# Kernel tuning notes

Hardware: AMD Instinct MI355X
Metric: run time of the kernel (lower is better)

Reference implementation:

```python
import jax, jax.numpy as jnp
import numpy as np

N, E = 100000, 1600000
IN_F, H, D = 128, 4, 32
NEG_SLOPE = 0.2


def setup_inputs() -> dict:
    key = jax.random.key(0)
    k1, k2, k3, k4, k5, k6 = jax.random.split(key, 6)
    feat = jax.random.normal(k1, (N, IN_F), dtype=jnp.float32)
    src = jax.random.randint(k2, (E,), 0, N, dtype=jnp.int32)
    dst = jax.random.randint(k3, (E,), 0, N, dtype=jnp.int32)
    # learned params (xavier-ish scale)
    W = jax.random.normal(k4, (IN_F, H * D), dtype=jnp.float32) * (2.0 / (IN_F + H * D)) ** 0.5
    attn_l = jax.random.normal(k5, (H, D), dtype=jnp.float32) * 0.1
    attn_r = jax.random.normal(k6, (H, D), dtype=jnp.float32) * 0.1
    return {"feat": feat, "W": W, "attn_l": attn_l, "attn_r": attn_r, "src": src, "dst": dst}


def reference(feat, W, attn_l, attn_r, src, dst):
    n = feat.shape[0]
    # linear projection: [N, H, D]
    ft = (feat @ W).reshape(n, H, D)
    # per-node attention logits: [N, H]
    el = jnp.einsum('nhd,hd->nh', ft, attn_l)
    er = jnp.einsum('nhd,hd->nh', ft, attn_r)
    # per-edge score e_ij = LeakyReLU(el[src] + er[dst]): [E, H]
    e = el[src] + er[dst]
    e = jnp.where(e > 0, e, NEG_SLOPE * e)
    # edge softmax over incoming edges of each destination node
    emax = jax.ops.segment_max(e, dst, num_segments=n)        # [N, H]
    emax = jnp.where(jnp.isfinite(emax), emax, 0.0)           # guard isolated nodes
    ex = jnp.exp(e - emax[dst])                               # [E, H]
    denom = jax.ops.segment_sum(ex, dst, num_segments=n)      # [N, H]
    denom = jnp.where(denom > 0, denom, 1.0)
    a = ex / denom[dst]                                       # [E, H]
    # weighted gather-scatter aggregation: sum_j a_ij * ft_j
    m = ft[src] * a[:, :, None]                               # [E, H, D]
    rst = jax.ops.segment_sum(m, dst, num_segments=n)         # [N, H, D]
    return rst
```

## Files before the change

kernel.cpp:

```cpp
#include <hip/hip_runtime.h>
#include <hip/hip_fp16.h>

constexpr int IN_F = 128;
constexpr int NH   = 4;
constexpr int ND   = 32;
constexpr int HD   = 128;
constexpr float NEG_SLOPE = 0.2f;
constexpr int NBLK   = 256;
constexpr int BSH    = 7;
constexpr int BNODES = 1 << BSH;

using short8 = __attribute__((ext_vector_type(8))) short;
using f32x4  = __attribute__((ext_vector_type(4))) float;
using f32x2  = __attribute__((ext_vector_type(2))) float;

__device__ inline unsigned bf16b(float f) {
  unsigned u = __float_as_uint(f);
  return (u + 0x7FFFu + ((u >> 16) & 1u)) >> 16;
}

__global__ __launch_bounds__(256) void k_chist(
    const int* __restrict__ dst, int* __restrict__ cnt, int ne, int nbuk,
    const float* __restrict__ W, const float* __restrict__ attn_l,
    const float* __restrict__ attn_r, unsigned* __restrict__ wtx) {
  const int t = threadIdx.x;
  const int item = blockIdx.x * 256 + t;
  if (item < 144 * 16) {
    const int r = item >> 4, s = item & 15;
    const int k0 = s * 8;
    unsigned pk[4];
    if (r < HD) {
#pragma unroll
      for (int j2 = 0; j2 < 4; ++j2) {
        const unsigned lo = bf16b(W[(size_t)(k0 + 2 * j2) * HD + r]);
        const unsigned hi = bf16b(W[(size_t)(k0 + 2 * j2 + 1) * HD + r]);
        pk[j2] = lo | (hi << 16);
      }
    } else if (r < HD + 8) {
      const int j8 = r - HD;
      const int h = j8 & 3;
      const float* av = (j8 < 4 ? attn_l : attn_r) + h * ND;
      float sums[8];
#pragma unroll
      for (int j = 0; j < 8; ++j) {
        const float4* wv = (const float4*)&W[(size_t)(k0 + j) * HD + h * ND];
        const float4* a4 = (const float4*)av;
        float sum = 0.f;
#pragma unroll
        for (int c4 = 0; c4 < ND / 4; ++c4) {
          const float4 w = wv[c4], a = a4[c4];
          sum += w.x * a.x + w.y * a.y + w.z * a.z + w.w * a.w;
        }
        sums[j] = sum;
      }
#pragma unroll
      for (int j2 = 0; j2 < 4; ++j2)
        pk[j2] = bf16b(sums[2 * j2]) | (bf16b(sums[2 * j2 + 1]) << 16);
    } else {
      pk[0] = pk[1] = pk[2] = pk[3] = 0;
    }
    *(uint4*)&wtx[r * 64 + ((s ^ (r & 7)) << 2)] =
        make_uint4(pk[0], pk[1], pk[2], pk[3]);
  }
  __shared__ int hist[1024];
  for (int b = t; b < nbuk; b += 256) hist[b] = 0;
  __syncthreads();
  const int chunk = (ne + NBLK - 1) / NBLK;
  const int start = blockIdx.x * chunk;
  const int end = min(start + chunk, ne);
  for (int e = start + t; e < end; e += 256)
    atomicAdd(&hist[dst[e] >> BSH], 1);
  __syncthreads();
  for (int b = t; b < nbuk; b += 256) cnt[b * NBLK + blockIdx.x] = hist[b];
}

__global__ __launch_bounds__(256) void k_gemm(
    const float* __restrict__ feat, const unsigned* __restrict__ wtx,
    unsigned* __restrict__ ftb2, float* __restrict__ el, float* __restrict__ er,
    int n) {
  __shared__ unsigned sB[144 * 64];
  const int t = threadIdx.x;
  {
    const uint4* wx = (const uint4*)wtx;
    uint4* sx = (uint4*)sB;
    for (int it = t; it < 144 * 16; it += 256) sx[it] = wx[it];
  }
  __syncthreads();

  const int lane = t & 63;
  const int wv   = t >> 6;
  const int r0   = blockIdx.x * 128 + wv * 32;
  if (r0 >= n) return;
  const int lrow = lane & 15;
  const int lk   = lane >> 4;

  f32x4 acc[2][9];
#pragma unroll
  for (int st = 0; st < 2; ++st)
#pragma unroll
    for (int ct = 0; ct < 9; ++ct) acc[st][ct] = (f32x4)0.f;

#pragma unroll
  for (int ks = 0; ks < 4; ++ks) {
    short8 b[9];
#pragma unroll
    for (int ct = 0; ct < 9; ++ct) {
      const int row = ct * 16 + lrow;
      const int slot = ks * 4 + lk;
      b[ct] = *(const short8*)&sB[row * 64 + ((slot ^ (row & 7)) << 2)];
    }
#pragma unroll
    for (int st = 0; st < 2; ++st) {
      int arow = r0 + st * 16 + lrow;
      arow = arow < n ? arow : n - 1;
      const float* ap = feat + (size_t)arow * IN_F + ks * 32 + lk * 8;
      const float4 f0 = *(const float4*)ap;
      const float4 f1 = *(const float4*)(ap + 4);
      short8 a;
      a[0] = (short)bf16b(f0.x); a[1] = (short)bf16b(f0.y);
      a[2] = (short)bf16b(f0.z); a[3] = (short)bf16b(f0.w);
      a[4] = (short)bf16b(f1.x); a[5] = (short)bf16b(f1.y);
      a[6] = (short)bf16b(f1.z); a[7] = (short)bf16b(f1.w);
#pragma unroll
      for (int ct = 0; ct < 9; ++ct)
        acc[st][ct] = __builtin_amdgcn_mfma_f32_16x16x32_bf16(a, b[ct], acc[st][ct], 0, 0, 0);
    }
  }

#pragma unroll
  for (int st = 0; st < 2; ++st) {
#pragma unroll
    for (int i = 0; i < 4; ++i) {
      const int r = r0 + st * 16 + lk * 4 + i;
      if (r >= n) continue;
#pragma unroll
      for (int ct = 0; ct < 4; ++ct) {
        const unsigned pk = bf16b(acc[st][ct][i]) | (bf16b(acc[st][ct + 4][i]) << 16);
        ftb2[(size_t)r * 64 + ct * 16 + lrow] = pk;
      }
      if (lrow < 4)      el[r * NH + lrow]     = acc[st][8][i];
      else if (lrow < 8) er[r * NH + lrow - 4] = acc[st][8][i];
    }
  }
}

__global__ __launch_bounds__(256) void k_scan1(
    const int* __restrict__ in, int* __restrict__ pexcl,
    int* __restrict__ bsum, int len) {
  const int t = threadIdx.x;
  const int base = blockIdx.x * 1024 + t * 4;
  int v0 = base + 0 < len ? in[base + 0] : 0;
  int v1 = base + 1 < len ? in[base + 1] : 0;
  int v2 = base + 2 < len ? in[base + 2] : 0;
  int v3 = base + 3 < len ? in[base + 3] : 0;
  const int s = v0 + v1 + v2 + v3;
  const int lane = t & 63, w = t >> 6;
  int x = s;
#pragma unroll
  for (int off = 1; off < 64; off <<= 1) {
    int y = __shfl_up(x, off);
    if (lane >= off) x += y;
  }
  __shared__ int ws[4];
  if (lane == 63) ws[w] = x;
  __syncthreads();
  int woff = 0;
  for (int i = 0; i < w; ++i) woff += ws[i];
  int run = woff + x - s;
  if (base + 0 < len) { pexcl[base + 0] = run; run += v0; }
  if (base + 1 < len) { pexcl[base + 1] = run; run += v1; }
  if (base + 2 < len) { pexcl[base + 2] = run; run += v2; }
  if (base + 3 < len) { pexcl[base + 3] = run; run += v3; }
  if (t == 0) bsum[blockIdx.x] = ws[0] + ws[1] + ws[2] + ws[3];
}

__global__ __launch_bounds__(256) void k_scan23(
    const int* __restrict__ pexcl, const int* __restrict__ bsum,
    int* __restrict__ outv, int B, int len) {
  const int t = threadIdx.x;
  const int s = t < B ? bsum[t] : 0;
  const int lane = t & 63, w = t >> 6;
  int x = s;
#pragma unroll
  for (int off = 1; off < 64; off <<= 1) {
    int y = __shfl_up(x, off);
    if (lane >= off) x += y;
  }
  __shared__ int ws[4];
  __shared__ int sboff[256];
  if (lane == 63) ws[w] = x;
  __syncthreads();
  int woff = 0;
  for (int i = 0; i < w; ++i) woff += ws[i];
  sboff[t] = woff + x - s;
  __syncthreads();
  const int myoff = sboff[blockIdx.x];
  const int base = blockIdx.x * 1024 + t * 4;
#pragma unroll
  for (int j = 0; j < 4; ++j)
    if (base + j < len) outv[base + j] = pexcl[base + j] + myoff;
}

__global__ __launch_bounds__(256) void k_part(
    const int* __restrict__ src, const int* __restrict__ dst,
    const int* __restrict__ scanned, int2* __restrict__ pair, int ne, int nbuk) {
  __shared__ int cur[1024];
  const int t = threadIdx.x;
  for (int b = t; b < nbuk; b += 256) cur[b] = scanned[b * NBLK + blockIdx.x];
  __syncthreads();
  const int chunk = (ne + NBLK - 1) / NBLK;
  const int start = blockIdx.x * chunk;
  const int end = min(start + chunk, ne);
  for (int e = start + t; e < end; e += 256) {
    const int d = dst[e];
    const int pos = atomicAdd(&cur[d >> BSH], 1);
    pair[pos] = make_int2(src[e], d);
  }
}

__global__ __launch_bounds__(256) void k_fsort(
    const int2* __restrict__ pair, const int* __restrict__ scanned,
    const float* __restrict__ el, const float* __restrict__ er,
    int* __restrict__ offsets, int4* __restrict__ rec,
    int n, int ne, int nbuk) {
  const int b = blockIdx.x;
  const int t = threadIdx.x;
  const int base = scanned[b * NBLK];
  const int endp = (b + 1 < nbuk) ? scanned[(b + 1) * NBLK] : ne;
  __shared__ int hist[BNODES];
  __shared__ int cur[BNODES];
  __shared__ int ws2[2];
  if (t < BNODES) hist[t] = 0;
  __syncthreads();
  for (int i = base + t; i < endp; i += 256)
    atomicAdd(&hist[pair[i].y & (BNODES - 1)], 1);
  __syncthreads();
  int x = 0, v = 0;
  if (t < BNODES) {
    v = hist[t];
    x = v;
    const int lane = t & 63;
#pragma unroll
    for (int off = 1; off < 64; off <<= 1) {
      int y = __shfl_up(x, off);
      if (lane >= off) x += y;
    }
    if (lane == 63) ws2[t >> 6] = x;
  }
  __syncthreads();
  if (t < BNODES) {
    if (t >= 64) x += ws2[0];
    const int excl = base + x - v;
    cur[t] = excl;
    const int node = (b << BSH) + t;
    if (node < n) offsets[node] = excl;
  }
  if (b == 0 && t == 0) offsets[n] = ne;
  __syncthreads();
  for (int i = base + t; i < endp; i += 256) {
    const int2 pr = pair[i];
    const int pos = atomicAdd(&cur[pr.y & (BNODES - 1)], 1);
    const float4 l = *(const float4*)(el + (size_t)pr.x * NH);
    const float4 r = *(const float4*)(er + (size_t)pr.y * NH);
    float e0 = l.x + r.x, e1 = l.y + r.y, e2 = l.z + r.z, e3 = l.w + r.w;
    e0 = e0 > 0.f ? e0 : NEG_SLOPE * e0;
    e1 = e1 > 0.f ? e1 : NEG_SLOPE * e1;
    e2 = e2 > 0.f ? e2 : NEG_SLOPE * e2;
    e3 = e3 > 0.f ? e3 : NEG_SLOPE * e3;
    const __half2 h02 = __float22half2_rn(make_float2(__expf(e0), __expf(e2)));
    const __half2 h13 = __float22half2_rn(make_float2(__expf(e1), __expf(e3)));
    int4 rc;
    rc.x = pr.x;
    rc.y = *(const int*)&h02;
    rc.z = pr.x;
    rc.w = *(const int*)&h13;
    rec[pos] = rc;
  }
}

__global__ __launch_bounds__(256) void k_aggr(
    const int* __restrict__ offsets, const int* __restrict__ rec,
    const unsigned* __restrict__ ftb2, float* __restrict__ out, int n) {
  const int t = threadIdx.x;
  const int lane = t & 63;
  const int gw = (blockIdx.x * 256 + t) >> 6;
  const int q = lane >> 4;
  const int c = lane & 15;
  const int hsel = c >> 3;
  const int node = gw * 4 + q;
  int start = 0, end = 0;
  if (node < n) { start = offsets[node]; end = offsets[node + 1]; }
  int md = end - start;
  md = max(md, __shfl_xor(md, 16));
  md = max(md, __shfl_xor(md, 32));
  const char* recb = (const char*)rec + (hsel << 3);
  const unsigned* fb = ftb2 + (c << 2);

  f32x2 acc0 = {0.f, 0.f}, acc1 = {0.f, 0.f};
  f32x2 acc2 = {0.f, 0.f}, acc3 = {0.f, 0.f};
  f32x2 den  = {0.f, 0.f};

  for (int it = 0; it < md; it += 4) {
    int2 r[4];
#pragma unroll
    for (int k = 0; k < 4; ++k) {
      const int idx = start + it + k;
      int cl = min(idx, end - 1);
      cl = cl < 0 ? 0 : cl;
      r[k] = *(const int2*)(recb + ((size_t)cl << 4));
      if (idx >= end) r[k].y = 0;
    }
#pragma unroll
    for (int k = 0; k < 4; ++k) {
      const uint4 v = *(const uint4*)(fb + (size_t)r[k].x * 64);
      const float2 pf = __half22float2(*(const __half2*)&r[k].y);
      f32x2 p; p.x = pf.x; p.y = pf.y;
      f32x2 f;
      f.x = __uint_as_float(v.x << 16);
      f.y = __uint_as_float(v.x & 0xFFFF0000u);
      asm("v_pk_fma_f32 %0, %1, %2, %0" : "+v"(acc0) : "v"(f), "v"(p));
      f.x = __uint_as_float(v.y << 16);
      f.y = __uint_as_float(v.y & 0xFFFF0000u);
      asm("v_pk_fma_f32 %0, %1, %2, %0" : "+v"(acc1) : "v"(f), "v"(p));
      f.x = __uint_as_float(v.z << 16);
      f.y = __uint_as_float(v.z & 0xFFFF0000u);
      asm("v_pk_fma_f32 %0, %1, %2, %0" : "+v"(acc2) : "v"(f), "v"(p));
      f.x = __uint_as_float(v.w << 16);
      f.y = __uint_as_float(v.w & 0xFFFF0000u);
      asm("v_pk_fma_f32 %0, %1, %2, %0" : "+v"(acc3) : "v"(f), "v"(p));
      asm("v_pk_add_f32 %0, %1, %0" : "+v"(den) : "v"(p));
    }
  }

  if (node < n) {
    const float d0 = den.x > 0.f ? den.x : 1.f;
    const float d1 = den.y > 0.f ? den.y : 1.f;
    const float r0 = __builtin_amdgcn_rcpf(d0);
    const float r1 = __builtin_amdgcn_rcpf(d1);
    float* orow = out + (size_t)node * HD;
    *(float4*)(orow + (c << 2)) =
        make_float4(acc0.x * r0, acc1.x * r0, acc2.x * r0, acc3.x * r0);
    *(float4*)(orow + 64 + (c << 2)) =
        make_float4(acc0.y * r1, acc1.y * r1, acc2.y * r1, acc3.y * r1);
  }
}

extern "C" void kernel_launch(void* const* d_in, const int* in_sizes, int n_in,
                              void* d_out, int out_size, void* d_ws, size_t ws_size,
                              hipStream_t stream) {
  const float* feat   = (const float*)d_in[0];
  const float* W      = (const float*)d_in[1];
  const float* attn_l = (const float*)d_in[2];
  const float* attn_r = (const float*)d_in[3];
  const int*   src    = (const int*)d_in[4];
  const int*   dst    = (const int*)d_in[5];
  const int n  = in_sizes[0] / IN_F;
  const int ne = in_sizes[4];
  float* out = (float*)d_out;

  const int nbuk = (n + BNODES - 1) >> BSH;
  const int tbl  = nbuk * NBLK;
  const int Bt   = (tbl + 1023) / 1024;

  char* wp = (char*)d_ws;
  unsigned* ftb2 = (unsigned*)wp; wp += (size_t)n * 64 * 4;
  int4*  rec     = (int4*)wp;     wp += (size_t)ne * 16;
  int2*  pair    = (int2*)wp;     wp += (size_t)ne * 8;
  unsigned* wtx  = (unsigned*)wp; wp += (size_t)144 * 64 * 4;
  float* el      = (float*)wp;    wp += (size_t)n * NH * 4;
  float* er      = (float*)wp;    wp += (size_t)n * NH * 4;
  int*   cnt     = (int*)wp;      wp += (size_t)tbl * 4;
  int*   pexcl   = (int*)wp;      wp += (size_t)tbl * 4;
  int*   scanned = (int*)wp;      wp += (size_t)tbl * 4;
  int*   offsets = (int*)wp;      wp += (size_t)(n + 1) * 4;
  int*   bsum    = (int*)wp;      wp += 256 * 4;

  k_chist<<<NBLK, 256, 0, stream>>>(dst, cnt, ne, nbuk, W, attn_l, attn_r, wtx);
  k_gemm<<<(n + 127) / 128, 256, 0, stream>>>(feat, wtx, ftb2, el, er, n);
  k_scan1<<<Bt, 256, 0, stream>>>(cnt, pexcl, bsum, tbl);
  k_scan23<<<Bt, 256, 0, stream>>>(pexcl, bsum, scanned, Bt, tbl);
  k_part<<<NBLK, 256, 0, stream>>>(src, dst, scanned, pair, ne, nbuk);
  k_fsort<<<nbuk, 256, 0, stream>>>(pair, scanned, el, er, offsets, rec, n, ne, nbuk);
  k_aggr<<<(n + 15) / 16, 256, 0, stream>>>(offsets, (const int*)rec, ftb2, out, n);
}
```

Baseline: 156.1 us.

## Fuse edge partition into GEMM kernel and pack partitioned pairs into one word

The edge-partition pass now runs inside the projection GEMM kernel: the first NBLK blocks scatter edges after finishing their GEMM tile, which removes one launch and lets partitioning share the GPU with the matmul. Partitioned pairs shrink from an int2 to a single 32-bit word holding src<<7 plus the destination's low bits, and the destination is rebuilt from the bucket index in k_fsort, halving that traffic. The packing relies on src fitting in 25 bits. The aggregation loop also now iterates per quarter-wave over each node's own edge range instead of the wave-wide maximum, so lanes in one wave take different trip counts.

```diff
diff --git a/kernel.cpp b/kernel.cpp
--- a/kernel.cpp
+++ b/kernel.cpp
@@ -74,76 +74,6 @@
   for (int b = t; b < nbuk; b += 256) cnt[b * NBLK + blockIdx.x] = hist[b];
 }
 
-__global__ __launch_bounds__(256) void k_gemm(
-    const float* __restrict__ feat, const unsigned* __restrict__ wtx,
-    unsigned* __restrict__ ftb2, float* __restrict__ el, float* __restrict__ er,
-    int n) {
-  __shared__ unsigned sB[144 * 64];
-  const int t = threadIdx.x;
-  {
-    const uint4* wx = (const uint4*)wtx;
-    uint4* sx = (uint4*)sB;
-    for (int it = t; it < 144 * 16; it += 256) sx[it] = wx[it];
-  }
-  __syncthreads();
-
-  const int lane = t & 63;
-  const int wv   = t >> 6;
-  const int r0   = blockIdx.x * 128 + wv * 32;
-  if (r0 >= n) return;
-  const int lrow = lane & 15;
-  const int lk   = lane >> 4;
-
-  f32x4 acc[2][9];
-#pragma unroll
-  for (int st = 0; st < 2; ++st)
-#pragma unroll
-    for (int ct = 0; ct < 9; ++ct) acc[st][ct] = (f32x4)0.f;
-
-#pragma unroll
-  for (int ks = 0; ks < 4; ++ks) {
-    short8 b[9];
-#pragma unroll
-    for (int ct = 0; ct < 9; ++ct) {
-      const int row = ct * 16 + lrow;
-      const int slot = ks * 4 + lk;
-      b[ct] = *(const short8*)&sB[row * 64 + ((slot ^ (row & 7)) << 2)];
-    }
-#pragma unroll
-    for (int st = 0; st < 2; ++st) {
-      int arow = r0 + st * 16 + lrow;
-      arow = arow < n ? arow : n - 1;
-      const float* ap = feat + (size_t)arow * IN_F + ks * 32 + lk * 8;
-      const float4 f0 = *(const float4*)ap;
-      const float4 f1 = *(const float4*)(ap + 4);
-      short8 a;
-      a[0] = (short)bf16b(f0.x); a[1] = (short)bf16b(f0.y);
-      a[2] = (short)bf16b(f0.z); a[3] = (short)bf16b(f0.w);
-      a[4] = (short)bf16b(f1.x); a[5] = (short)bf16b(f1.y);
-      a[6] = (short)bf16b(f1.z); a[7] = (short)bf16b(f1.w);
-#pragma unroll
-      for (int ct = 0; ct < 9; ++ct)
-        acc[st][ct] = __builtin_amdgcn_mfma_f32_16x16x32_bf16(a, b[ct], acc[st][ct], 0, 0, 0);
-    }
-  }
-
-#pragma unroll
-  for (int st = 0; st < 2; ++st) {
-#pragma unroll
-    for (int i = 0; i < 4; ++i) {
-      const int r = r0 + st * 16 + lk * 4 + i;
-      if (r >= n) continue;
-#pragma unroll
-      for (int ct = 0; ct < 4; ++ct) {
-        const unsigned pk = bf16b(acc[st][ct][i]) | (bf16b(acc[st][ct + 4][i]) << 16);
-        ftb2[(size_t)r * 64 + ct * 16 + lrow] = pk;
-      }
-      if (lrow < 4)      el[r * NH + lrow]     = acc[st][8][i];
-      else if (lrow < 8) er[r * NH + lrow - 4] = acc[st][8][i];
-    }
-  }
-}
-
 __global__ __launch_bounds__(256) void k_scan1(
     const int* __restrict__ in, int* __restrict__ pexcl,
     int* __restrict__ bsum, int len) {
@@ -201,25 +131,95 @@
     if (base + j < len) outv[base + j] = pexcl[base + j] + myoff;
 }
 
-__global__ __launch_bounds__(256) void k_part(
-    const int* __restrict__ src, const int* __restrict__ dst,
-    const int* __restrict__ scanned, int2* __restrict__ pair, int ne, int nbuk) {
+__global__ __launch_bounds__(256) void k_gemm(
+    const float* __restrict__ feat, const unsigned* __restrict__ wtx,
+    unsigned* __restrict__ ftb2, float* __restrict__ el, float* __restrict__ er,
+    int n, const int* __restrict__ src, const int* __restrict__ dst,
+    const int* __restrict__ scanned, unsigned* __restrict__ pairp,
+    int ne, int nbuk) {
+  __shared__ unsigned sB[144 * 64];
   __shared__ int cur[1024];
   const int t = threadIdx.x;
-  for (int b = t; b < nbuk; b += 256) cur[b] = scanned[b * NBLK + blockIdx.x];
-  __syncthreads();
-  const int chunk = (ne + NBLK - 1) / NBLK;
-  const int start = blockIdx.x * chunk;
-  const int end = min(start + chunk, ne);
-  for (int e = start + t; e < end; e += 256) {
-    const int d = dst[e];
-    const int pos = atomicAdd(&cur[d >> BSH], 1);
-    pair[pos] = make_int2(src[e], d);
+  {
+    const uint4* wx = (const uint4*)wtx;
+    uint4* sx = (uint4*)sB;
+    for (int it = t; it < 144 * 16; it += 256) sx[it] = wx[it];
+  }
+  __syncthreads();
+
+  const int lane = t & 63;
+  const int wv   = t >> 6;
+  const int r0   = blockIdx.x * 128 + wv * 32;
+  const int lrow = lane & 15;
+  const int lk   = lane >> 4;
+
+  if (r0 < n) {
+    f32x4 acc[2][9];
+#pragma unroll
+    for (int st = 0; st < 2; ++st)
+#pragma unroll
+      for (int ct = 0; ct < 9; ++ct) acc[st][ct] = (f32x4)0.f;
+
+#pragma unroll
+    for (int ks = 0; ks < 4; ++ks) {
+      short8 b[9];
+#pragma unroll
+      for (int ct = 0; ct < 9; ++ct) {
+        const int row = ct * 16 + lrow;
+        const int slot = ks * 4 + lk;
+        b[ct] = *(const short8*)&sB[row * 64 + ((slot ^ (row & 7)) << 2)];
+      }
+#pragma unroll
+      for (int st = 0; st < 2; ++st) {
+        int arow = r0 + st * 16 + lrow;
+        arow = arow < n ? arow : n - 1;
+        const float* ap = feat + (size_t)arow * IN_F + ks * 32 + lk * 8;
+        const float4 f0 = *(const float4*)ap;
+        const float4 f1 = *(const float4*)(ap + 4);
+        short8 a;
+        a[0] = (short)bf16b(f0.x); a[1] = (short)bf16b(f0.y);
+        a[2] = (short)bf16b(f0.z); a[3] = (short)bf16b(f0.w);
+        a[4] = (short)bf16b(f1.x); a[5] = (short)bf16b(f1.y);
+        a[6] = (short)bf16b(f1.z); a[7] = (short)bf16b(f1.w);
+#pragma unroll
+        for (int ct = 0; ct < 9; ++ct)
+          acc[st][ct] = __builtin_amdgcn_mfma_f32_16x16x32_bf16(a, b[ct], acc[st][ct], 0, 0, 0);
+      }
+    }
+
+#pragma unroll
+    for (int st = 0; st < 2; ++st) {
+#pragma unroll
+      for (int i = 0; i < 4; ++i) {
+        const int r = r0 + st * 16 + lk * 4 + i;
+        if (r >= n) continue;
+#pragma unroll
+        for (int ct = 0; ct < 4; ++ct) {
+          const unsigned pk = bf16b(acc[st][ct][i]) | (bf16b(acc[st][ct + 4][i]) << 16);
+          ftb2[(size_t)r * 64 + ct * 16 + lrow] = pk;
+        }
+        if (lrow < 4)      el[r * NH + lrow]     = acc[st][8][i];
+        else if (lrow < 8) er[r * NH + lrow - 4] = acc[st][8][i];
+      }
+    }
+  }
+
+  if (blockIdx.x < NBLK) {
+    for (int b = t; b < nbuk; b += 256) cur[b] = scanned[b * NBLK + blockIdx.x];
+    __syncthreads();
+    const int chunk = (ne + NBLK - 1) / NBLK;
+    const int start = blockIdx.x * chunk;
+    const int end = min(start + chunk, ne);
+    for (int e = start + t; e < end; e += 256) {
+      const int d = dst[e];
+      const int pos = atomicAdd(&cur[d >> BSH], 1);
+      pairp[pos] = ((unsigned)src[e] << BSH) | (unsigned)(d & (BNODES - 1));
+    }
   }
 }
 
 __global__ __launch_bounds__(256) void k_fsort(
-    const int2* __restrict__ pair, const int* __restrict__ scanned,
+    const unsigned* __restrict__ pair, const int* __restrict__ scanned,
     const float* __restrict__ el, const float* __restrict__ er,
     int* __restrict__ offsets, int4* __restrict__ rec,
     int n, int ne, int nbuk) {
@@ -233,7 +233,7 @@
   if (t < BNODES) hist[t] = 0;
   __syncthreads();
   for (int i = base + t; i < endp; i += 256)
-    atomicAdd(&hist[pair[i].y & (BNODES - 1)], 1);
+    atomicAdd(&hist[pair[i] & (BNODES - 1)], 1);
   __syncthreads();
   int x = 0, v = 0;
   if (t < BNODES) {
@@ -258,10 +258,13 @@
   if (b == 0 && t == 0) offsets[n] = ne;
   __syncthreads();
   for (int i = base + t; i < endp; i += 256) {
-    const int2 pr = pair[i];
-    const int pos = atomicAdd(&cur[pr.y & (BNODES - 1)], 1);
-    const float4 l = *(const float4*)(el + (size_t)pr.x * NH);
-    const float4 r = *(const float4*)(er + (size_t)pr.y * NH);
+    const unsigned pr = pair[i];
+    const int s = (int)(pr >> BSH);
+    const int fn = (int)(pr & (BNODES - 1));
+    const int d = (b << BSH) + fn;
+    const int pos = atomicAdd(&cur[fn], 1);
+    const float4 l = *(const float4*)(el + (size_t)s * NH);
+    const float4 r = *(const float4*)(er + (size_t)d * NH);
     float e0 = l.x + r.x, e1 = l.y + r.y, e2 = l.z + r.z, e3 = l.w + r.w;
     e0 = e0 > 0.f ? e0 : NEG_SLOPE * e0;
     e1 = e1 > 0.f ? e1 : NEG_SLOPE * e1;
@@ -270,9 +273,9 @@
     const __half2 h02 = __float22half2_rn(make_float2(__expf(e0), __expf(e2)));
     const __half2 h13 = __float22half2_rn(make_float2(__expf(e1), __expf(e3)));
     int4 rc;
-    rc.x = pr.x;
+    rc.x = s;
     rc.y = *(const int*)&h02;
-    rc.z = pr.x;
+    rc.z = s;
     rc.w = *(const int*)&h13;
     rec[pos] = rc;
   }
@@ -290,9 +293,6 @@
   const int node = gw * 4 + q;
   int start = 0, end = 0;
   if (node < n) { start = offsets[node]; end = offsets[node + 1]; }
-  int md = end - start;
-  md = max(md, __shfl_xor(md, 16));
-  md = max(md, __shfl_xor(md, 32));
   const char* recb = (const char*)rec + (hsel << 3);
   const unsigned* fb = ftb2 + (c << 2);
 
@@ -300,13 +300,12 @@
   f32x2 acc2 = {0.f, 0.f}, acc3 = {0.f, 0.f};
   f32x2 den  = {0.f, 0.f};
 
-  for (int it = 0; it < md; it += 4) {
+  for (int i = start; i < end; i += 4) {
     int2 r[4];
 #pragma unroll
     for (int k = 0; k < 4; ++k) {
-      const int idx = start + it + k;
-      int cl = min(idx, end - 1);
-      cl = cl < 0 ? 0 : cl;
+      const int idx = i + k;
+      const int cl = min(idx, end - 1);
       r[k] = *(const int2*)(recb + ((size_t)cl << 4));
       if (idx >= end) r[k].y = 0;
     }
@@ -365,7 +364,7 @@
   char* wp = (char*)d_ws;
   unsigned* ftb2 = (unsigned*)wp; wp += (size_t)n * 64 * 4;
   int4*  rec     = (int4*)wp;     wp += (size_t)ne * 16;
-  int2*  pair    = (int2*)wp;     wp += (size_t)ne * 8;
+  unsigned* pairp = (unsigned*)wp; wp += (size_t)ne * 4;
   unsigned* wtx  = (unsigned*)wp; wp += (size_t)144 * 64 * 4;
   float* el      = (float*)wp;    wp += (size_t)n * NH * 4;
   float* er      = (float*)wp;    wp += (size_t)n * NH * 4;
@@ -376,10 +375,10 @@
   int*   bsum    = (int*)wp;      wp += 256 * 4;
 
   k_chist<<<NBLK, 256, 0, stream>>>(dst, cnt, ne, nbuk, W, attn_l, attn_r, wtx);
-  k_gemm<<<(n + 127) / 128, 256, 0, stream>>>(feat, wtx, ftb2, el, er, n);
   k_scan1<<<Bt, 256, 0, stream>>>(cnt, pexcl, bsum, tbl);
   k_scan23<<<Bt, 256, 0, stream>>>(pexcl, bsum, scanned, Bt, tbl);
-  k_part<<<NBLK, 256, 0, stream>>>(src, dst, scanned, pair, ne, nbuk);
-  k_fsort<<<nbuk, 256, 0, stream>>>(pair, scanned, el, er, offsets, rec, n, ne, nbuk);
+  k_gemm<<<(n + 127) / 128, 256, 0, stream>>>(feat, wtx, ftb2, el, er, n,
+                                              src, dst, scanned, pairp, ne, nbuk);
+  k_fsort<<<nbuk, 256, 0, stream>>>(pairp, scanned, el, er, offsets, rec, n, ne, nbuk);
   k_aggr<<<(n + 15) / 16, 256, 0, stream>>>(offsets, (const int*)rec, ftb2, out, n);
 }
```

After: 144.4 us. 1.08x faster.
